# Optimization experiments

Measured on AMD Instinct MI355X. Metric: run time of the kernel, lower is better.

The kernel has to match this reference:

```python
import jax, jax.numpy as jnp
import numpy as np


def setup_inputs() -> dict:
    key = jax.random.key(0)
    ks = jax.random.split(key, 7)
    n, dim, h, d = 4096, 512, 8, 64
    return {
        "Q": jax.random.normal(ks[0], (n, dim), dtype=jnp.float32),
        "K": jax.random.normal(ks[1], (n, dim), dtype=jnp.float32),
        "V": jax.random.normal(ks[2], (n, dim), dtype=jnp.float32),
        "Wq": jax.random.uniform(ks[3], (h, dim, d), dtype=jnp.float32),
        "Wk": jax.random.uniform(ks[4], (h, dim, d), dtype=jnp.float32),
        "Wv": jax.random.uniform(ks[5], (h, dim, d), dtype=jnp.float32),
        "Wo": jax.random.uniform(ks[6], (dim, dim), dtype=jnp.float32),
    }


def reference(Q, K, V, Wq, Wk, Wv, Wo):
    # Per-head projections, vectorized over the head axis h.
    q = jnp.einsum("nd,hde->hne", Q, Wq)  # (h, n, d)
    k = jnp.einsum("md,hde->hme", K, Wk)  # (h, N, d)
    v = jnp.einsum("md,hde->hme", V, Wv)  # (h, N, d)
    d_k = Wq.shape[-1]
    scale = jnp.asarray(1.0 / np.sqrt(d_k), dtype=Q.dtype)
    scores = jnp.einsum("hne,hme->hnm", q, k) * scale  # (h, n, N)
    attn = jax.nn.softmax(scores, axis=-1)  # softmax over keys (row dim 1 of 2D input)
    out = jnp.einsum("hnm,hme->hne", attn, v)  # (h, n, d)
    # Concatenate heads along feature dim in head order, then output projection.
    n = Q.shape[0]
    out = jnp.transpose(out, (1, 0, 2)).reshape(n, -1)  # (n, h*d) == (n, dim)
    return out @ Wo
```

## Files before the change

kernel.cpp:

```cpp
#include <hip/hip_runtime.h>


typedef __attribute__((ext_vector_type(8))) short bf16x8;
typedef __attribute__((ext_vector_type(8))) _Float16 f16x8;
typedef __attribute__((ext_vector_type(4))) float f32x4;
typedef unsigned short u16;

static __device__ __forceinline__ u16 f2bf(float f) {
  union { float f; unsigned u; } v; v.f = f;
  unsigned r = v.u + 0x7fffu + ((v.u >> 16) & 1u);
  return (u16)(r >> 16);
}
static __device__ __forceinline__ float bf2f(u16 h) {
  union { unsigned u; float f; } v; v.u = ((unsigned)h) << 16; return v.f;
}
static __device__ __forceinline__ u16 f2h(float f) {
  union { _Float16 h; u16 u; } v; v.h = (_Float16)f; return v.u;
}
static __device__ __forceinline__ unsigned cvt_pk_bf16(float lo, float hi) {
  unsigned r;
  asm("v_cvt_pk_bf16_f32 %0, %1, %2" : "=v"(r) : "v"(lo), "v"(hi));
  return r;
}
static __device__ __forceinline__ float exp2a(float x) {
  float r;
  asm("v_exp_f32 %0, %1" : "=v"(r) : "v"(x));
  return r;
}
static __device__ __forceinline__ void split2(float v0, float v1,
                                              unsigned& hw, unsigned& lw) {
  unsigned h = cvt_pk_bf16(v0, v1);
  float h0 = __uint_as_float(h << 16);
  float h1 = __uint_as_float(h & 0xffff0000u);
  hw = h;
  lw = cvt_pk_bf16(v0 - h0, v1 - h1);
}

#define MAX3(a, b, c) fmaxf(fmaxf(a, b), c)

#define SWZ(row, byteoff) ((((row) * 128) + (byteoff)) ^ (((row) & 7) << 4))

static __device__ __forceinline__ int sigma64(int k) {
  return (k & 3) | (((k >> 5) & 1) << 2) | (((k >> 2) & 3) << 3) | (((k >> 4) & 1) << 5);
}

#define GLOAD16(gp, lp)                                              \
  __builtin_amdgcn_global_load_lds(                                  \
      (const __attribute__((address_space(1))) void*)(gp),           \
      (__attribute__((address_space(3))) void*)(lp), 16, 0, 0)

__global__ __launch_bounds__(256) void prep_weights(const float* __restrict__ Wq,
                                                    const float* __restrict__ Wk,
                                                    const float* __restrict__ Wv,
                                                    const float* __restrict__ Wo,
                                                    u16* __restrict__ Wall_h,
                                                    u16* __restrict__ Wall_l,
                                                    u16* __restrict__ WoTp) {
  int i = blockIdx.x * 256 + threadIdx.x;
  if (i < 786432) {
    int which = i / 262144, rem = i - which * 262144;
    int b = rem >> 15, r2 = rem & 32767;
    int c = r2 >> 9, r = r2 & 511;
    const float* W = which == 0 ? Wq : which == 1 ? Wk : Wv;
    float x = W[(b << 15) + r * 64 + c];
    u16 h = f2bf(x);
    size_t off = (size_t)(which * 8 + b) * 32768 +
                 (size_t)((r >> 5) * 4 + (c >> 4)) * 512 +
                 ((((r & 31) >> 3) * 16) + (c & 15)) * 8 + (r & 7);
    Wall_h[off] = h;
    Wall_l[off] = f2bf(x - bf2f(h));
  } else if (i < 786432 + 262144) {
    int rem = i - 786432;
    int c = rem >> 9, r = rem & 511;
    size_t off = (size_t)(c >> 6) * 32768 +
                 (size_t)((r >> 5) * 4 + ((c >> 4) & 3)) * 512 +
                 ((((r & 31) >> 3) * 16) + (c & 15)) * 8 + (r & 7);
    WoTp[off] = f2bf(Wo[r * 512 + c]);
  }
}

__global__ __launch_bounds__(256) void proj_gemm(const float* __restrict__ Q,
                                                 const float* __restrict__ Kin,
                                                 const float* __restrict__ Vin,
                                                 const u16* __restrict__ Wall_h,
                                                 const u16* __restrict__ Wall_l,
                                                 u16* __restrict__ qh,
                                                 u16* __restrict__ khg,
                                                 u16* __restrict__ vsg) {
  const int n = 4096, K = 512, N = 64;
  int rb = blockIdx.x;
  int which = blockIdx.y >> 3, b = blockIdx.y & 7;
  int wave = threadIdx.x >> 6, lane = threadIdx.x & 63;
  int lr = lane & 15, lg = lane >> 4;
  int row0 = rb * 64 + wave * 16;

  const float* A = which == 0 ? Q : which == 1 ? Kin : Vin;
  const u16* Bh = Wall_h + (size_t)(which * 8 + b) * 32768 + lane * 8;
  const u16* Bl = Wall_l + (size_t)(which * 8 + b) * 32768 + lane * 8;

  const float* Arow = A + (size_t)(row0 + lr) * K + lg * 8;

  union U8 { unsigned w[4]; bf16x8 v; };
  f32x4 acc[4] = {};

  float4 a0 = *(const float4*)(Arow);
  float4 a1 = *(const float4*)(Arow + 4);
  bf16x8 bh[4], bl[4];
#pragma unroll
  for (int ct = 0; ct < 4; ++ct) bh[ct] = *(const bf16x8*)(Bh + ct * 512);
  if (which != 2) {
#pragma unroll
    for (int ct = 0; ct < 4; ++ct) bl[ct] = *(const bf16x8*)(Bl + ct * 512);
  }

#pragma unroll
  for (int ks = 0; ks < 16; ++ks) {
    float4 a0n, a1n;
    bf16x8 bhn[4], bln[4];
    if (ks < 15) {
      a0n = *(const float4*)(Arow + (ks + 1) * 32);
      a1n = *(const float4*)(Arow + (ks + 1) * 32 + 4);
#pragma unroll
      for (int ct = 0; ct < 4; ++ct)
        bhn[ct] = *(const bf16x8*)(Bh + ((ks + 1) * 4 + ct) * 512);
      if (which != 2) {
#pragma unroll
        for (int ct = 0; ct < 4; ++ct)
          bln[ct] = *(const bf16x8*)(Bl + ((ks + 1) * 4 + ct) * 512);
      }
    }
    U8 ah, al;
    split2(a0.x, a0.y, ah.w[0], al.w[0]);
    split2(a0.z, a0.w, ah.w[1], al.w[1]);
    split2(a1.x, a1.y, ah.w[2], al.w[2]);
    split2(a1.z, a1.w, ah.w[3], al.w[3]);
#pragma unroll
    for (int ct = 0; ct < 4; ++ct)
      acc[ct] = __builtin_amdgcn_mfma_f32_16x16x32_bf16(ah.v, bh[ct], acc[ct], 0, 0, 0);
    if (which != 2) {
#pragma unroll
      for (int ct = 0; ct < 4; ++ct) {
        acc[ct] = __builtin_amdgcn_mfma_f32_16x16x32_bf16(al.v, bh[ct], acc[ct], 0, 0, 0);
        acc[ct] = __builtin_amdgcn_mfma_f32_16x16x32_bf16(ah.v, bl[ct], acc[ct], 0, 0, 0);
      }
    }
    if (ks < 15) {
      a0 = a0n; a1 = a1n;
#pragma unroll
      for (int ct = 0; ct < 4; ++ct) bh[ct] = bhn[ct];
      if (which != 2) {
#pragma unroll
        for (int ct = 0; ct < 4; ++ct) bl[ct] = bln[ct];
      }
    }
  }

  const float QSCALE = 0.125f * 1.44269504f;
#pragma unroll
  for (int ct = 0; ct < 4; ++ct)
#pragma unroll
    for (int r = 0; r < 4; ++r) {
      float v = acc[ct][r];
      int row = row0 + lg * 4 + r;
      int col = ct * 16 + lr;
      if (which == 2) {
        size_t byte = ((size_t)b * 64 + (row >> 6)) * 8192 +
                      SWZ(col, 2 * sigma64(row & 63));
        *(u16*)((char*)vsg + byte) = f2bf(v);
      } else if (which == 1) {
        size_t byte = ((size_t)b * 64 + (row >> 6)) * 8192 + SWZ(row & 63, col * 2);
        *(u16*)((char*)khg + byte) = f2h(v);
      } else {
        qh[((size_t)b * n + row) * N + col] = f2h(v * QSCALE);
      }
    }
}

__global__ __launch_bounds__(256, 4) void attn_kernel(const u16* __restrict__ qh,
                                                      const u16* __restrict__ khg,
                                                      const u16* __restrict__ vsg,
                                                      u16* __restrict__ Opart,
                                                      float2* __restrict__ ml) {
  const int n = 4096, d = 64;
  int bid = blockIdx.x;
  int j = bid & 7, w = bid >> 3;
  int grp = j * 4 + (w >> 5);
  int qb = w & 31;
  int h = grp >> 2, part = grp & 3;
  int wave = threadIdx.x >> 6, lane = threadIdx.x & 63;
  int c = lane & 15, g = lane >> 4;

  __shared__ char SB[32768];

  int qrow0 = qb * 128 + wave * 32;
  f16x8 qf[2][2];
#pragma unroll
  for (int b2 = 0; b2 < 2; ++b2)
#pragma unroll
    for (int ks = 0; ks < 2; ++ks) {
      size_t qoff = ((size_t)h * n + qrow0 + b2 * 16 + c) * d + ks * 32 + g * 8;
      qf[b2][ks] = *(const f16x8*)(qh + qoff);
    }

  int koff[4][2];
#pragma unroll
  for (int ct = 0; ct < 4; ++ct)
#pragma unroll
    for (int ks = 0; ks < 2; ++ks)
      koff[ct][ks] = SWZ(ct * 16 + c, ks * 64 + g * 16);

  union { unsigned w[4]; bf16x8 v; } ones;
  ones.w[0] = 0x3f803f80u; ones.w[1] = 0x3f803f80u;
  ones.w[2] = 0x3f803f80u; ones.w[3] = 0x3f803f80u;

  f32x4 accO[2][4] = {};
  f32x4 accL[2] = {};
  float m[2] = {-INFINITY, -INFINITY};

  const char* khB = (const char*)khg + ((size_t)h * 64 + part * 16) * 8192;
  const char* vsB = (const char*)vsg + ((size_t)h * 64 + part * 16) * 8192;
  int so = wave * 2048;
  int sg = so + lane * 16;

#define STAGE(tile, BUF)                                            \
  do {                                                              \
    const char* kg_ = khB + (size_t)(tile) * 8192 + sg;             \
    const char* vg_ = vsB + (size_t)(tile) * 8192 + sg;             \
    char* kd_ = SB + (BUF)*8192 + so;                               \
    char* vd_ = SB + 16384 + (BUF)*8192 + so;                       \
    GLOAD16(kg_, kd_);                                              \
    GLOAD16(kg_ + 1024, kd_ + 1024);                                \
    GLOAD16(vg_, vd_);                                              \
    GLOAD16(vg_ + 1024, vd_ + 1024);                                \
  } while (0)

#define TILE(IT, CUR)                                                          \
  do {                                                                         \
    asm volatile("s_waitcnt vmcnt(0)" ::: "memory");                           \
    __builtin_amdgcn_s_barrier();                                              \
    asm volatile("" ::: "memory");                                             \
    if ((IT) < 15) STAGE((IT) + 1, 1 - (CUR));                                 \
    f32x4 s[2][4] = {};                                                        \
    __builtin_amdgcn_s_setprio(1);                                             \
    _Pragma("unroll") for (int ct = 0; ct < 4; ++ct) {                         \
      _Pragma("unroll") for (int ks = 0; ks < 2; ++ks) {                       \
        f16x8 kf = *(const f16x8*)(SB + (CUR)*8192 + koff[ct][ks]);            \
        s[0][ct] = __builtin_amdgcn_mfma_f32_16x16x32_f16(kf, qf[0][ks],       \
                                                          s[0][ct], 0, 0, 0);  \
        s[1][ct] = __builtin_amdgcn_mfma_f32_16x16x32_f16(kf, qf[1][ks],       \
                                                          s[1][ct], 0, 0, 0);  \
      }                                                                        \
    }                                                                          \
    __builtin_amdgcn_s_setprio(0);                                             \
    float mxv[2];                                                              \
    _Pragma("unroll") for (int b2 = 0; b2 < 2; ++b2) {                         \
      float t0 = MAX3(s[b2][0][0], s[b2][0][1], s[b2][0][2]);                  \
      float t1 = MAX3(s[b2][0][3], s[b2][1][0], s[b2][1][1]);                  \
      float t2 = MAX3(s[b2][1][2], s[b2][1][3], s[b2][2][0]);                  \
      float t3 = MAX3(s[b2][2][1], s[b2][2][2], s[b2][2][3]);                  \
      float t4 = MAX3(s[b2][3][0], s[b2][3][1], s[b2][3][2]);                  \
      mxv[b2] = fmaxf(MAX3(t0, t1, t2), MAX3(t3, t4, s[b2][3][3]));            \
    }                                                                          \
    _Pragma("unroll") for (int b2 = 0; b2 < 2; ++b2)                           \
        mxv[b2] = fmaxf(mxv[b2], __shfl_xor(mxv[b2], 16));                     \
    _Pragma("unroll") for (int b2 = 0; b2 < 2; ++b2)                           \
        mxv[b2] = fmaxf(mxv[b2], __shfl_xor(mxv[b2], 32));                     \
    _Pragma("unroll") for (int b2 = 0; b2 < 2; ++b2) {                         \
      bool need = mxv[b2] > m[b2] + 8.0f;         \
      float mn = need ? mxv[b2] : m[b2];                                       \
      _Pragma("unroll") for (int ct = 0; ct < 4; ++ct) {                       \
        s[b2][ct][0] = exp2a(s[b2][ct][0] - mn);                               \
        s[b2][ct][1] = exp2a(s[b2][ct][1] - mn);                               \
        s[b2][ct][2] = exp2a(s[b2][ct][2] - mn);                               \
        s[b2][ct][3] = exp2a(s[b2][ct][3] - mn);                               \
      }                                                                        \
      if (__any(need)) {                                                       \
        float alpha = exp2a(m[b2] - mn);                                       \
        m[b2] = mn;                                                            \
        _Pragma("unroll") for (int r = 0; r < 4; ++r) {                        \
          float ar = __shfl(alpha, g * 4 + r);                                 \
          accL[b2][r] *= ar;                                                   \
          _Pragma("unroll") for (int dt = 0; dt < 4; ++dt)                     \
              accO[b2][dt][r] *= ar;                                           \
        }                                                                      \
      }                                                                        \
    }                                                                          \
    union { unsigned w[4]; bf16x8 v; } pa[2][2];                               \
    _Pragma("unroll") for (int b2 = 0; b2 < 2; ++b2)                           \
        _Pragma("unroll") for (int ks = 0; ks < 2; ++ks) {                     \
      pa[b2][ks].w[0] = cvt_pk_bf16(s[b2][ks][0], s[b2][ks][1]);               \
      pa[b2][ks].w[1] = cvt_pk_bf16(s[b2][ks][2], s[b2][ks][3]);               \
      pa[b2][ks].w[2] = cvt_pk_bf16(s[b2][ks + 2][0], s[b2][ks + 2][1]);       \
      pa[b2][ks].w[3] = cvt_pk_bf16(s[b2][ks + 2][2], s[b2][ks + 2][3]);       \
    }                                                                          \
    __builtin_amdgcn_s_setprio(1);                                             \
    _Pragma("unroll") for (int dt = 0; dt < 4; ++dt) {                         \
      _Pragma("unroll") for (int ks = 0; ks < 2; ++ks) {                       \
        bf16x8 vf =                                                            \
            *(const bf16x8*)(SB + 16384 + (CUR)*8192 + koff[dt][ks]);          \
        accO[0][dt] = __builtin_amdgcn_mfma_f32_16x16x32_bf16(                 \
            pa[0][ks].v, vf, accO[0][dt], 0, 0, 0);                            \
        accO[1][dt] = __builtin_amdgcn_mfma_f32_16x16x32_bf16(                 \
            pa[1][ks].v, vf, accO[1][dt], 0, 0, 0);                            \
      }                                                                        \
    }                                                                          \
    accL[0] = __builtin_amdgcn_mfma_f32_16x16x32_bf16(pa[0][0].v, ones.v,      \
                                                      accL[0], 0, 0, 0);       \
    accL[0] = __builtin_amdgcn_mfma_f32_16x16x32_bf16(pa[0][1].v, ones.v,      \
                                                      accL[0], 0, 0, 0);       \
    accL[1] = __builtin_amdgcn_mfma_f32_16x16x32_bf16(pa[1][0].v, ones.v,      \
                                                      accL[1], 0, 0, 0);       \
    accL[1] = __builtin_amdgcn_mfma_f32_16x16x32_bf16(pa[1][1].v, ones.v,      \
                                                      accL[1], 0, 0, 0);       \
    __builtin_amdgcn_s_setprio(0);                                             \
  } while (0)

  STAGE(0, 0);
#pragma unroll 1
  for (int it2 = 0; it2 < 8; ++it2) {
    TILE(it2 * 2, 0);
    TILE(it2 * 2 + 1, 1);
  }
#undef TILE
#undef STAGE

  u16* Ob = Opart + (((size_t)part * 8 + h) * n) * d;
  float2* mlp = ml + ((size_t)part * 8 + h) * n;
#pragma unroll
  for (int b2 = 0; b2 < 2; ++b2) {
#pragma unroll
    for (int r = 0; r < 4; ++r) {
      int row = qrow0 + b2 * 16 + g * 4 + r;
#pragma unroll
      for (int dt = 0; dt < 4; ++dt)
        Ob[(size_t)row * d + dt * 16 + c] = f2bf(accO[b2][dt][r]);
      float mrow = __shfl(m[b2], g * 4 + r);
      if (c == 0)
        mlp[qrow0 + b2 * 16 + g * 4 + r] = make_float2(mrow, accL[b2][r]);
    }
  }
}

__global__ __launch_bounds__(256) void attn_combine(const u16* __restrict__ Opart,
                                                    const float2* __restrict__ ml,
                                                    u16* __restrict__ att) {
  int tid = blockIdx.x * 256 + threadIdx.x;
  int chunk = tid & 7;
  int h = (tid >> 3) & 7;
  int row = tid >> 6;
  float2 mls[4];
  float mstar = -INFINITY;
#pragma unroll
  for (int p = 0; p < 4; ++p) {
    mls[p] = ml[((size_t)p * 8 + h) * 4096 + row];
    mstar = fmaxf(mstar, mls[p].x);
  }
  float w[4], denom = 0.f;
#pragma unroll
  for (int p = 0; p < 4; ++p) {
    w[p] = exp2a(mls[p].x - mstar);
    denom += mls[p].y * w[p];
  }
  float inv = 1.f / denom;
  float res[8] = {};
#pragma unroll
  for (int p = 0; p < 4; ++p) {
    bf16x8 o = *(const bf16x8*)(Opart + (((size_t)p * 8 + h) * 4096 + row) * 64 + chunk * 8);
    float wp = w[p] * inv;
#pragma unroll
    for (int jj = 0; jj < 8; ++jj) res[jj] += bf2f((u16)o[jj]) * wp;
  }
  bf16x8 rv;
#pragma unroll
  for (int jj = 0; jj < 8; ++jj) rv[jj] = (short)f2bf(res[jj]);
  *(bf16x8*)(att + (size_t)row * 512 + h * 64 + chunk * 8) = rv;
}

__global__ __launch_bounds__(256) void final_gemm(const u16* __restrict__ A,
                                                  const u16* __restrict__ BTp,
                                                  float* __restrict__ out,
                                                  int M, int K, int N) {
  int rb = blockIdx.x, cb = blockIdx.y;
  int wave = threadIdx.x >> 6, lane = threadIdx.x & 63;
  int lr = lane & 15, lg = lane >> 4;
  int row0 = rb * 64 + wave * 16;

  const u16* Arow = A + (size_t)(row0 + lr) * K + lg * 8;
  const u16* Bp = BTp + (size_t)cb * 32768 + lane * 8;

  f32x4 acc[4] = {};
  bf16x8 a = *(const bf16x8*)(Arow);
  bf16x8 bfr[4];
#pragma unroll
  for (int ct = 0; ct < 4; ++ct) bfr[ct] = *(const bf16x8*)(Bp + ct * 512);

#pragma unroll
  for (int ks = 0; ks < 16; ++ks) {
    bf16x8 an, bfn[4];
    if (ks < 15) {
      an = *(const bf16x8*)(Arow + (ks + 1) * 32);
#pragma unroll
      for (int ct = 0; ct < 4; ++ct)
        bfn[ct] = *(const bf16x8*)(Bp + ((ks + 1) * 4 + ct) * 512);
    }
#pragma unroll
    for (int ct = 0; ct < 4; ++ct)
      acc[ct] = __builtin_amdgcn_mfma_f32_16x16x32_bf16(a, bfr[ct], acc[ct], 0, 0, 0);
    if (ks < 15) {
      a = an;
#pragma unroll
      for (int ct = 0; ct < 4; ++ct) bfr[ct] = bfn[ct];
    }
  }
#pragma unroll
  for (int ct = 0; ct < 4; ++ct)
#pragma unroll
    for (int r = 0; r < 4; ++r)
      out[(size_t)(row0 + lg * 4 + r) * N + cb * 64 + ct * 16 + lr] = acc[ct][r];
}

extern "C" void kernel_launch(void* const* d_in, const int* in_sizes, int n_in,
                              void* d_out, int out_size, void* d_ws, size_t ws_size,
                              hipStream_t stream) {
  const float* Q = (const float*)d_in[0];
  const float* K = (const float*)d_in[1];
  const float* V = (const float*)d_in[2];
  const float* Wq = (const float*)d_in[3];
  const float* Wk = (const float*)d_in[4];
  const float* Wv = (const float*)d_in[5];
  const float* Wo = (const float*)d_in[6];
  float* out = (float*)d_out;

  const int n = 4096, dim = 512;
  const size_t KB = 1 << 10, MB = 1 << 20;
  char* ws = (char*)d_ws;
  u16* qh     = (u16*)(ws + 0 * MB);
  u16* khg    = (u16*)(ws + 4 * MB);
  u16* vsg    = (u16*)(ws + 8 * MB);
  u16* Opart  = (u16*)(ws + 12 * MB);
  u16* Wall_h = (u16*)(ws + 12 * MB);
  u16* Wall_l = (u16*)(ws + 12 * MB + 1536 * KB);
  float2* ml  = (float2*)(ws + 28 * MB);
  u16* WoTp   = (u16*)(ws + 29 * MB);
  u16* att    = khg;

  prep_weights<<<4096, 256, 0, stream>>>(Wq, Wk, Wv, Wo, Wall_h, Wall_l, WoTp);

  proj_gemm<<<dim3(n / 64, 24), 256, 0, stream>>>(Q, K, V, Wall_h, Wall_l,
                                                  qh, khg, vsg);

  attn_kernel<<<1024, 256, 0, stream>>>(qh, khg, vsg, Opart, ml);
  attn_combine<<<(n * 8 * 8) / 256, 256, 0, stream>>>(Opart, ml, att);

  final_gemm<<<dim3(n / 64, dim / 64), 256, 0, stream>>>(att, WoTp, out, n, dim, dim);
}
```

Before: 117.8 us.

## Use fp16 weights with two-term fp16 activation split in projection GEMM

The projection GEMM drops the bf16 three-product split (hi*hi, lo*hi, hi*lo with separate hi/lo weight arrays) in favour of a single fp16 copy of each weight and a two-term fp16 split of the activations. That cuts the weight-side MFMAs and weight loads. Each wave now covers 32 rows instead of 16, reusing the weight fragments across two row tiles and halving the grid. Loads are prefetched three stages deep. The final GEMM also gets a four-stage prefetch ring. Accuracy now relies on fp16 range and mantissa for the weights and activation pieces, and the V projection now does two MFMAs per tile where it used to do one.

Result: faster. 105.0 us (-10.8%).

```diff
diff --git a/kernel.cpp b/kernel.cpp
--- a/kernel.cpp
+++ b/kernel.cpp
@@ -27,13 +27,18 @@
   asm("v_exp_f32 %0, %1" : "=v"(r) : "v"(x));
   return r;
 }
-static __device__ __forceinline__ void split2(float v0, float v1,
-                                              unsigned& hw, unsigned& lw) {
-  unsigned h = cvt_pk_bf16(v0, v1);
-  float h0 = __uint_as_float(h << 16);
-  float h1 = __uint_as_float(h & 0xffff0000u);
-  hw = h;
-  lw = cvt_pk_bf16(v0 - h0, v1 - h1);
+
+static __device__ __forceinline__ void split8_f16(float4 p, float4 q,
+                                                  f16x8& hi, f16x8& lo) {
+  float a[8] = {p.x, p.y, p.z, p.w, q.x, q.y, q.z, q.w};
+  union { _Float16 h[8]; f16x8 v; } H, L;
+#pragma unroll
+  for (int i = 0; i < 8; ++i) {
+    float th = __uint_as_float(__float_as_uint(a[i]) & 0xffffe000u);
+    H.h[i] = (_Float16)th;
+    L.h[i] = (_Float16)(a[i] - th);
+  }
+  hi = H.v; lo = L.v;
 }
 
 #define MAX3(a, b, c) fmaxf(fmaxf(a, b), c)
@@ -53,8 +58,7 @@
                                                     const float* __restrict__ Wk,
                                                     const float* __restrict__ Wv,
                                                     const float* __restrict__ Wo,
-                                                    u16* __restrict__ Wall_h,
-                                                    u16* __restrict__ Wall_l,
+                                                    u16* __restrict__ Wall,
                                                     u16* __restrict__ WoTp) {
   int i = blockIdx.x * 256 + threadIdx.x;
   if (i < 786432) {
@@ -63,12 +67,10 @@
     int c = r2 >> 9, r = r2 & 511;
     const float* W = which == 0 ? Wq : which == 1 ? Wk : Wv;
     float x = W[(b << 15) + r * 64 + c];
-    u16 h = f2bf(x);
     size_t off = (size_t)(which * 8 + b) * 32768 +
                  (size_t)((r >> 5) * 4 + (c >> 4)) * 512 +
                  ((((r & 31) >> 3) * 16) + (c & 15)) * 8 + (r & 7);
-    Wall_h[off] = h;
-    Wall_l[off] = f2bf(x - bf2f(h));
+    Wall[off] = f2h(x);
   } else if (i < 786432 + 262144) {
     int rem = i - 786432;
     int c = rem >> 9, r = rem & 511;
@@ -82,8 +84,7 @@
 __global__ __launch_bounds__(256) void proj_gemm(const float* __restrict__ Q,
                                                  const float* __restrict__ Kin,
                                                  const float* __restrict__ Vin,
-                                                 const u16* __restrict__ Wall_h,
-                                                 const u16* __restrict__ Wall_l,
+                                                 const u16* __restrict__ Wall,
                                                  u16* __restrict__ qh,
                                                  u16* __restrict__ khg,
                                                  u16* __restrict__ vsg) {
@@ -92,88 +93,75 @@
   int which = blockIdx.y >> 3, b = blockIdx.y & 7;
   int wave = threadIdx.x >> 6, lane = threadIdx.x & 63;
   int lr = lane & 15, lg = lane >> 4;
-  int row0 = rb * 64 + wave * 16;
+  int row0 = rb * 128 + wave * 32;
 
   const float* A = which == 0 ? Q : which == 1 ? Kin : Vin;
-  const u16* Bh = Wall_h + (size_t)(which * 8 + b) * 32768 + lane * 8;
-  const u16* Bl = Wall_l + (size_t)(which * 8 + b) * 32768 + lane * 8;
-
-  const float* Arow = A + (size_t)(row0 + lr) * K + lg * 8;
-
-  union U8 { unsigned w[4]; bf16x8 v; };
-  f32x4 acc[4] = {};
-
-  float4 a0 = *(const float4*)(Arow);
-  float4 a1 = *(const float4*)(Arow + 4);
-  bf16x8 bh[4], bl[4];
-#pragma unroll
-  for (int ct = 0; ct < 4; ++ct) bh[ct] = *(const bf16x8*)(Bh + ct * 512);
-  if (which != 2) {
-#pragma unroll
-    for (int ct = 0; ct < 4; ++ct) bl[ct] = *(const bf16x8*)(Bl + ct * 512);
+  const u16* Bp = Wall + (size_t)(which * 8 + b) * 32768 + lane * 8;
+  const float* Ar0 = A + (size_t)(row0 + lr) * K + lg * 8;
+  const float* Ar1 = Ar0 + (size_t)16 * K;
+
+  f32x4 acc[2][4] = {};
+
+  float4 ax[3][4];
+  f16x8 bw[3][4];
+#pragma unroll
+  for (int p = 0; p < 3; ++p) {
+    ax[p][0] = *(const float4*)(Ar0 + p * 32);
+    ax[p][1] = *(const float4*)(Ar0 + p * 32 + 4);
+    ax[p][2] = *(const float4*)(Ar1 + p * 32);
+    ax[p][3] = *(const float4*)(Ar1 + p * 32 + 4);
+#pragma unroll
+    for (int ct = 0; ct < 4; ++ct)
+      bw[p][ct] = *(const f16x8*)(Bp + (p * 4 + ct) * 512);
   }
 
 #pragma unroll
   for (int ks = 0; ks < 16; ++ks) {
-    float4 a0n, a1n;
-    bf16x8 bhn[4], bln[4];
-    if (ks < 15) {
-      a0n = *(const float4*)(Arow + (ks + 1) * 32);
-      a1n = *(const float4*)(Arow + (ks + 1) * 32 + 4);
+    int s = ks % 3;
+    f16x8 ah0, al0, ah1, al1;
+    split8_f16(ax[s][0], ax[s][1], ah0, al0);
+    split8_f16(ax[s][2], ax[s][3], ah1, al1);
+    if (ks < 13) {
+      ax[s][0] = *(const float4*)(Ar0 + (ks + 3) * 32);
+      ax[s][1] = *(const float4*)(Ar0 + (ks + 3) * 32 + 4);
+      ax[s][2] = *(const float4*)(Ar1 + (ks + 3) * 32);
+      ax[s][3] = *(const float4*)(Ar1 + (ks + 3) * 32 + 4);
+    }
+#pragma unroll
+    for (int ct = 0; ct < 4; ++ct) {
+      acc[0][ct] = __builtin_amdgcn_mfma_f32_16x16x32_f16(ah0, bw[s][ct], acc[0][ct], 0, 0, 0);
+      acc[0][ct] = __builtin_amdgcn_mfma_f32_16x16x32_f16(al0, bw[s][ct], acc[0][ct], 0, 0, 0);
+      acc[1][ct] = __builtin_amdgcn_mfma_f32_16x16x32_f16(ah1, bw[s][ct], acc[1][ct], 0, 0, 0);
+      acc[1][ct] = __builtin_amdgcn_mfma_f32_16x16x32_f16(al1, bw[s][ct], acc[1][ct], 0, 0, 0);
+    }
+    if (ks < 13) {
 #pragma unroll
       for (int ct = 0; ct < 4; ++ct)
-        bhn[ct] = *(const bf16x8*)(Bh + ((ks + 1) * 4 + ct) * 512);
-      if (which != 2) {
-#pragma unroll
-        for (int ct = 0; ct < 4; ++ct)
-          bln[ct] = *(const bf16x8*)(Bl + ((ks + 1) * 4 + ct) * 512);
+        bw[s][ct] = *(const f16x8*)(Bp + ((ks + 3) * 4 + ct) * 512);
+    }
+  }
+
+  const float QSCALE = 0.125f * 1.44269504f;
+#pragma unroll
+  for (int b2 = 0; b2 < 2; ++b2)
+#pragma unroll
+    for (int ct = 0; ct < 4; ++ct)
+#pragma unroll
+      for (int r = 0; r < 4; ++r) {
+        float v = acc[b2][ct][r];
+        int row = row0 + b2 * 16 + lg * 4 + r;
+        int col = ct * 16 + lr;
+        if (which == 2) {
+          size_t byte = ((size_t)b * 64 + (row >> 6)) * 8192 +
+                        SWZ(col, 2 * sigma64(row & 63));
+          *(u16*)((char*)vsg + byte) = f2bf(v);
+        } else if (which == 1) {
+          size_t byte = ((size_t)b * 64 + (row >> 6)) * 8192 + SWZ(row & 63, col * 2);
+          *(u16*)((char*)khg + byte) = f2h(v);
+        } else {
+          qh[((size_t)b * n + row) * N + col] = f2h(v * QSCALE);
+        }
       }
-    }
-    U8 ah, al;
-    split2(a0.x, a0.y, ah.w[0], al.w[0]);
-    split2(a0.z, a0.w, ah.w[1], al.w[1]);
-    split2(a1.x, a1.y, ah.w[2], al.w[2]);
-    split2(a1.z, a1.w, ah.w[3], al.w[3]);
-#pragma unroll
-    for (int ct = 0; ct < 4; ++ct)
-      acc[ct] = __builtin_amdgcn_mfma_f32_16x16x32_bf16(ah.v, bh[ct], acc[ct], 0, 0, 0);
-    if (which != 2) {
-#pragma unroll
-      for (int ct = 0; ct < 4; ++ct) {
-        acc[ct] = __builtin_amdgcn_mfma_f32_16x16x32_bf16(al.v, bh[ct], acc[ct], 0, 0, 0);
-        acc[ct] = __builtin_amdgcn_mfma_f32_16x16x32_bf16(ah.v, bl[ct], acc[ct], 0, 0, 0);
-      }
-    }
-    if (ks < 15) {
-      a0 = a0n; a1 = a1n;
-#pragma unroll
-      for (int ct = 0; ct < 4; ++ct) bh[ct] = bhn[ct];
-      if (which != 2) {
-#pragma unroll
-        for (int ct = 0; ct < 4; ++ct) bl[ct] = bln[ct];
-      }
-    }
-  }
-
-  const float QSCALE = 0.125f * 1.44269504f;
-#pragma unroll
-  for (int ct = 0; ct < 4; ++ct)
-#pragma unroll
-    for (int r = 0; r < 4; ++r) {
-      float v = acc[ct][r];
-      int row = row0 + lg * 4 + r;
-      int col = ct * 16 + lr;
-      if (which == 2) {
-        size_t byte = ((size_t)b * 64 + (row >> 6)) * 8192 +
-                      SWZ(col, 2 * sigma64(row & 63));
-        *(u16*)((char*)vsg + byte) = f2bf(v);
-      } else if (which == 1) {
-        size_t byte = ((size_t)b * 64 + (row >> 6)) * 8192 + SWZ(row & 63, col * 2);
-        *(u16*)((char*)khg + byte) = f2h(v);
-      } else {
-        qh[((size_t)b * n + row) * N + col] = f2h(v * QSCALE);
-      }
-    }
 }
 
 __global__ __launch_bounds__(256, 4) void attn_kernel(const u16* __restrict__ qh,
@@ -389,27 +377,27 @@
   const u16* Bp = BTp + (size_t)cb * 32768 + lane * 8;
 
   f32x4 acc[4] = {};
-  bf16x8 a = *(const bf16x8*)(Arow);
-  bf16x8 bfr[4];
-#pragma unroll
-  for (int ct = 0; ct < 4; ++ct) bfr[ct] = *(const bf16x8*)(Bp + ct * 512);
+  bf16x8 a[4];
+  bf16x8 bb[4][4];
+#pragma unroll
+  for (int p = 0; p < 4; ++p) {
+    a[p] = *(const bf16x8*)(Arow + p * 32);
+#pragma unroll
+    for (int ct = 0; ct < 4; ++ct)
+      bb[p][ct] = *(const bf16x8*)(Bp + (p * 4 + ct) * 512);
+  }
 
 #pragma unroll
   for (int ks = 0; ks < 16; ++ks) {
-    bf16x8 an, bfn[4];
-    if (ks < 15) {
-      an = *(const bf16x8*)(Arow + (ks + 1) * 32);
+    int s = ks & 3;
+#pragma unroll
+    for (int ct = 0; ct < 4; ++ct)
+      acc[ct] = __builtin_amdgcn_mfma_f32_16x16x32_bf16(a[s], bb[s][ct], acc[ct], 0, 0, 0);
+    if (ks < 12) {
+      a[s] = *(const bf16x8*)(Arow + (ks + 4) * 32);
 #pragma unroll
       for (int ct = 0; ct < 4; ++ct)
-        bfn[ct] = *(const bf16x8*)(Bp + ((ks + 1) * 4 + ct) * 512);
-    }
-#pragma unroll
-    for (int ct = 0; ct < 4; ++ct)
-      acc[ct] = __builtin_amdgcn_mfma_f32_16x16x32_bf16(a, bfr[ct], acc[ct], 0, 0, 0);
-    if (ks < 15) {
-      a = an;
-#pragma unroll
-      for (int ct = 0; ct < 4; ++ct) bfr[ct] = bfn[ct];
+        bb[s][ct] = *(const bf16x8*)(Bp + ((ks + 4) * 4 + ct) * 512);
     }
   }
 #pragma unroll
@@ -438,16 +426,14 @@
   u16* khg    = (u16*)(ws + 4 * MB);
   u16* vsg    = (u16*)(ws + 8 * MB);
   u16* Opart  = (u16*)(ws + 12 * MB);
-  u16* Wall_h = (u16*)(ws + 12 * MB);
-  u16* Wall_l = (u16*)(ws + 12 * MB + 1536 * KB);
+  u16* Wall   = (u16*)(ws + 12 * MB);
   float2* ml  = (float2*)(ws + 28 * MB);
   u16* WoTp   = (u16*)(ws + 29 * MB);
   u16* att    = khg;
 
-  prep_weights<<<4096, 256, 0, stream>>>(Wq, Wk, Wv, Wo, Wall_h, Wall_l, WoTp);
-
-  proj_gemm<<<dim3(n / 64, 24), 256, 0, stream>>>(Q, K, V, Wall_h, Wall_l,
-                                                  qh, khg, vsg);
+  prep_weights<<<4096, 256, 0, stream>>>(Wq, Wk, Wv, Wo, Wall, WoTp);
+
+  proj_gemm<<<dim3(32, 24), 256, 0, stream>>>(Q, K, V, Wall, qh, khg, vsg);
 
   attn_kernel<<<1024, 256, 0, stream>>>(qh, khg, vsg, Opart, ml);
   attn_combine<<<(n * 8 * 8) / 256, 256, 0, stream>>>(Opart, ml, att);
```
